# Kernel tuning notes

Measured on AMD Instinct MI355X. Metric: run time of the kernel, lower is better.

Reference implementation:

```python
import jax, jax.numpy as jnp
import numpy as np

N, E, F, H, C, K = 50000, 1600000, 128, 64, 40, 4


def setup_inputs() -> dict:
    key = jax.random.key(0)
    ks = jax.random.split(key, 4)
    x = jax.random.normal(ks[0], (N, F), dtype=jnp.float32)
    edge_index = jax.random.randint(ks[1], (2, E), 0, N, dtype=jnp.int32)
    edge_weight = jnp.ones((E,), dtype=jnp.float32)
    # lin of ChebConv: Linear(K*in, out); kaiming for layer1, xavier-ish for layer2
    W1 = jax.random.normal(ks[2], (K * F, H), dtype=jnp.float32) * (2.0 / (K * F)) ** 0.5
    b1 = jnp.zeros((H,), jnp.float32)
    W2 = jax.random.normal(ks[3], (K * H, C), dtype=jnp.float32) * (2.0 / (K * H + C)) ** 0.5
    b2 = jnp.zeros((C,), jnp.float32)
    return {"x": x, "edge_index": edge_index, "edge_weight": edge_weight,
            "W1": W1, "b1": b1, "W2": W2, "b2": b2}


def _cheb_norm(edge_index, edge_weight, num_nodes):
    """Edge weights of L_hat = 2*L/lambda_max - I with sym norm, lambda_max=2.
    L = I - D^{-1/2} A D^{-1/2}; so L_hat off-diag = -d_i^{-1/2} w d_j^{-1/2},
    diag = (1 if deg>0 else 0) - 1."""
    src, dst = edge_index[0], edge_index[1]
    deg = jax.ops.segment_sum(edge_weight, src, num_segments=num_nodes)
    dis = jnp.where(deg > 0, jax.lax.rsqrt(jnp.maximum(deg, 1e-12)), 0.0)
    w_norm = -dis[src] * edge_weight * dis[dst]   # [E] off-diagonal of L_hat
    diag = jnp.where(deg > 0, 0.0, -1.0)          # [N] diagonal of L_hat
    return src, dst, w_norm, diag


def _cheb_conv(x, src, dst, w_norm, diag, W, b, num_nodes):
    def prop(h):  # L_hat @ h via gather-multiply-scatter
        msg = w_norm[:, None] * h[src]                                  # [E, F]
        return diag[:, None] * h + jax.ops.segment_sum(msg, dst, num_segments=num_nodes)

    Tx_prev2 = x
    Tx_prev1 = prop(x)
    Txs = [Tx_prev2, Tx_prev1]
    for _ in range(2, K):
        Tx = 2.0 * prop(Tx_prev1) - Tx_prev2
        Txs.append(Tx)
        Tx_prev2, Tx_prev1 = Tx_prev1, Tx
    Z = jnp.concatenate(Txs, axis=1)              # [N, K*F]
    return Z @ W + b


def reference(x, edge_index, edge_weight, W1, b1, W2, b2):
    num_nodes = x.shape[0]
    src, dst, w_norm, diag = _cheb_norm(edge_index, edge_weight, num_nodes)
    # dropout layers are identity at inference
    h = _cheb_conv(x, src, dst, w_norm, diag, W1, b1, num_nodes)
    h = jax.nn.relu(h)
    out = _cheb_conv(h, src, dst, w_norm, diag, W2, b2, num_nodes)
    return out
```

## Files before the change

### kernel.cpp

```cpp
#include <hip/hip_runtime.h>

#define NN 50000
#define EE 1600000
#define FF 128
#define HH 64
#define CC 40
#define NB 196

#define NCH 64
#define CHE (EE / NCH)
#define NSL 4
#define SLN (NN / NSL)
#define NCHF 16
#define CHEF (EE / NCHF)
#define NSLF 16
#define SLNF (NN / NSLF)

static __device__ __forceinline__ float bf2f(unsigned short u) {
    union { unsigned int i; float f; } c; c.i = ((unsigned int)u) << 16; return c.f;
}
static __device__ __forceinline__ unsigned short f2bf(float x) {
    union { float f; unsigned int i; } c; c.f = x;
    unsigned int r = c.i + 0x7FFFu + ((c.i >> 16) & 1u);
    return (unsigned short)(r >> 16);
}

__global__ __launch_bounds__(1024) void hist_kernel(
    const int* __restrict__ src, const int* __restrict__ dst,
    const float* __restrict__ w,
    float* __restrict__ pdeg, unsigned short* __restrict__ pcnt64) {
    __shared__ float        ldeg[SLN];
    __shared__ unsigned int lcnt[SLN / 2];
    int s = blockIdx.x % NSL;
    int c = blockIdx.x / NSL;
    int base = s * SLN;
    for (int i = threadIdx.x; i < SLN; i += 1024) ldeg[i] = 0.f;
    for (int i = threadIdx.x; i < SLN / 2; i += 1024) lcnt[i] = 0u;
    __syncthreads();
    int e0 = c * CHE;
    for (int e = e0 + threadIdx.x; e < e0 + CHE; e += 1024) {
        int se = src[e], de = dst[e];
        unsigned us = (unsigned)(se - base), ud = (unsigned)(de - base);
        if (us < SLN) atomicAdd(&ldeg[us], w[e]);
        if (ud < SLN) atomicAdd(&lcnt[ud >> 1], 1u << (16 * (ud & 1)));
    }
    __syncthreads();
    for (int i = threadIdx.x; i < SLN; i += 1024) {
        pdeg[(size_t)c * NN + base + i] = ldeg[i];
        pcnt64[(size_t)c * NN + base + i] =
            (unsigned short)((lcnt[i >> 1] >> (16 * (i & 1))) & 0xFFFFu);
    }
}

__global__ void reduce_kernel(const float* __restrict__ pdeg,
                              const unsigned short* __restrict__ pcnt64,
                              int* __restrict__ pcnt16, int* __restrict__ cnt,
                              float* __restrict__ dis, float* __restrict__ diag) {
    int n = blockIdx.x * blockDim.x + threadIdx.x;
    if (n >= NN) return;
    float dsum = 0.f;
    for (int c = 0; c < NCH; ++c) dsum += pdeg[(size_t)c * NN + n];
    int run = 0;
    for (int c16 = 0; c16 < NCHF; ++c16) {
        pcnt16[(size_t)c16 * NN + n] = run;
        #pragma unroll
        for (int q = 0; q < 4; ++q)
            run += pcnt64[(size_t)(c16 * 4 + q) * NN + n];
    }
    cnt[n] = run;
    dis[n]  = (dsum > 0.f) ? rsqrtf(fmaxf(dsum, 1e-12f)) : 0.f;
    diag[n] = (dsum > 0.f) ? 0.f : -1.f;
}

__global__ void scanA_kernel(const int* __restrict__ cnt, int* __restrict__ bsum) {
    __shared__ int sh[256];
    int i = blockIdx.x * 256 + threadIdx.x;
    sh[threadIdx.x] = (i < NN) ? cnt[i] : 0;
    __syncthreads();
    for (int off = 128; off > 0; off >>= 1) {
        if (threadIdx.x < off) sh[threadIdx.x] += sh[threadIdx.x + off];
        __syncthreads();
    }
    if (threadIdx.x == 0) bsum[blockIdx.x] = sh[0];
}

__global__ void scanB_kernel(const int* __restrict__ bsum, int* __restrict__ boff,
                             int* __restrict__ row_start) {
    if (threadIdx.x == 0) {
        int run = 0;
        for (int b = 0; b < NB; ++b) { boff[b] = run; run += bsum[b]; }
        row_start[NN] = run;
    }
}

__global__ void scanC_kernel(const int* __restrict__ cnt, const int* __restrict__ boff,
                             int* __restrict__ row_start) {
    __shared__ int sh[256];
    int t = threadIdx.x;
    int i = blockIdx.x * 256 + t;
    int v = (i < NN) ? cnt[i] : 0;
    sh[t] = v;
    __syncthreads();
    for (int off = 1; off < 256; off <<= 1) {
        int x = (t >= off) ? sh[t - off] : 0;
        __syncthreads();
        sh[t] += x;
        __syncthreads();
    }
    if (i < NN) row_start[i] = boff[blockIdx.x] + sh[t] - v;
}

__global__ __launch_bounds__(1024) void fill_kernel(
    const int* __restrict__ src, const int* __restrict__ dst,
    const float* __restrict__ w, const float* __restrict__ dis,
    const int* __restrict__ row_start, const int* __restrict__ pcnt16,
    unsigned int* __restrict__ csr) {
    __shared__ unsigned int lcur[(SLNF + 1) / 2];
    int s = blockIdx.x % NSLF;
    int c = blockIdx.x / NSLF;
    int base = s * SLNF;
    for (int i = threadIdx.x; i < (SLNF + 1) / 2; i += 1024) lcur[i] = 0u;
    __syncthreads();
    int e0 = c * CHEF;
    for (int e = e0 + threadIdx.x; e < e0 + CHEF; e += 1024) {
        int de = dst[e];
        unsigned ud = (unsigned)(de - base);
        if (ud < SLNF) {
            int se = src[e];
            unsigned sh = 16 * (ud & 1);
            unsigned old = atomicAdd(&lcur[ud >> 1], 1u << sh);
            int off = (int)((old >> sh) & 0xFFFFu);
            int pos = row_start[de] + pcnt16[(size_t)c * NN + de] + off;
            float wn = -dis[se] * w[e] * dis[de];
            unsigned int entry = (unsigned)se | ((unsigned)f2bf(wn) << 16);
            __builtin_nontemporal_store(entry, csr + pos);
        }
    }
}

template <int FACT, typename OUT_T>
__global__ __launch_bounds__(256) void prop2_kernel(
    const unsigned short* __restrict__ a, int aStride, float alphaL,
    const float* __restrict__ p1, float beta1,
    const float* __restrict__ p2, float beta2, int pStride,
    const float* __restrict__ bias, int doRelu, int FOUT, int outStride,
    const float* __restrict__ diag, const int* __restrict__ rs,
    const unsigned int* __restrict__ csr, OUT_T* __restrict__ out) {
    int lane = threadIdx.x & 63;
    int wave = threadIdx.x >> 6;
    int n = blockIdx.x * 4 + wave;
    int f = lane;
    float acc = 0.f;
    if (f < FACT) {
        acc = diag[n] * bf2f(a[(size_t)n * aStride + f]);
        int j0 = rs[n], j1 = rs[n + 1];
        int j = j0;
        for (; j + 8 <= j1; j += 8) {
            unsigned cw[8];
            #pragma unroll
            for (int u = 0; u < 8; ++u) cw[u] = csr[j + u];
            float v[8];
            #pragma unroll
            for (int u = 0; u < 8; ++u)
                v[u] = bf2f(a[(size_t)(cw[u] & 0xFFFFu) * aStride + f]);
            #pragma unroll
            for (int u = 0; u < 8; ++u)
                acc = fmaf(bf2f((unsigned short)(cw[u] >> 16)), v[u], acc);
        }
        for (; j < j1; ++j) {
            unsigned cw = csr[j];
            acc = fmaf(bf2f((unsigned short)(cw >> 16)),
                       bf2f(a[(size_t)(cw & 0xFFFFu) * aStride + f]), acc);
        }
    }
    if (f < FOUT) {
        float r = alphaL * acc + beta1 * p1[(size_t)n * pStride + f];
        if (beta2 != 0.f) r = fmaf(beta2, p2[(size_t)n * pStride + f], r);
        if (bias) r += bias[f];
        if (doRelu) r = fmaxf(r, 0.f);
        OUT_T o;
        if constexpr (sizeof(OUT_T) == 2) o = f2bf(r); else o = r;
        out[(size_t)n * outStride + f] = o;
    }
}

__global__ __launch_bounds__(256) void gemm1_kernel(
    const float* __restrict__ x, const float* __restrict__ W,
    float* __restrict__ Yf, unsigned short* __restrict__ y3b) {
    __shared__ float As[64][36];
    __shared__ float Bs[32][64];
    int t = threadIdx.x;
    int m0 = blockIdx.x * 64;
    int ct = blockIdx.y;
    int tr = t / 16, tc = t % 16;
    int kq = t % 8,  ms = t / 8;
    int jb = t % 16, fb = t / 16;
    float acc[4][4] = {};
    for (int kb = 0; kb < 4; ++kb) {
        __syncthreads();
        #pragma unroll
        for (int p = 0; p < 2; ++p) {
            int m = ms + 32 * p;
            int row = m0 + m;
            float4 vv = make_float4(0.f, 0.f, 0.f, 0.f);
            if (row < NN) vv = *(const float4*)(x + (size_t)row * FF + kb * 32 + kq * 4);
            *(float4*)&As[m][kq * 4] = vv;
        }
        const float* Wb = W + ((size_t)ct * 128 + kb * 32) * HH;
        #pragma unroll
        for (int p = 0; p < 2; ++p) {
            int fi = fb + 16 * p;
            float4 vv = *(const float4*)(Wb + fi * HH + jb * 4);
            *(float4*)&Bs[fi][jb * 4] = vv;
        }
        __syncthreads();
        #pragma unroll 8
        for (int k = 0; k < 32; ++k) {
            float a0 = As[tr * 4 + 0][k], a1 = As[tr * 4 + 1][k];
            float a2 = As[tr * 4 + 2][k], a3 = As[tr * 4 + 3][k];
            float4 b = *(float4*)&Bs[k][tc * 4];
            acc[0][0] = fmaf(a0, b.x, acc[0][0]); acc[0][1] = fmaf(a0, b.y, acc[0][1]);
            acc[0][2] = fmaf(a0, b.z, acc[0][2]); acc[0][3] = fmaf(a0, b.w, acc[0][3]);
            acc[1][0] = fmaf(a1, b.x, acc[1][0]); acc[1][1] = fmaf(a1, b.y, acc[1][1]);
            acc[1][2] = fmaf(a1, b.z, acc[1][2]); acc[1][3] = fmaf(a1, b.w, acc[1][3]);
            acc[2][0] = fmaf(a2, b.x, acc[2][0]); acc[2][1] = fmaf(a2, b.y, acc[2][1]);
            acc[2][2] = fmaf(a2, b.z, acc[2][2]); acc[2][3] = fmaf(a2, b.w, acc[2][3]);
            acc[3][0] = fmaf(a3, b.x, acc[3][0]); acc[3][1] = fmaf(a3, b.y, acc[3][1]);
            acc[3][2] = fmaf(a3, b.z, acc[3][2]); acc[3][3] = fmaf(a3, b.w, acc[3][3]);
        }
    }
    #pragma unroll
    for (int r = 0; r < 4; ++r) {
        int n = m0 + tr * 4 + r;
        if (n < NN) {
            *(float4*)(Yf + (size_t)n * 256 + ct * 64 + tc * 4) =
                make_float4(acc[r][0], acc[r][1], acc[r][2], acc[r][3]);
            if (ct == 3) {
                ushort4 u4;
                u4.x = f2bf(acc[r][0]); u4.y = f2bf(acc[r][1]);
                u4.z = f2bf(acc[r][2]); u4.w = f2bf(acc[r][3]);
                *(ushort4*)(y3b + (size_t)n * 64 + tc * 4) = u4;
            }
        }
    }
}

__global__ __launch_bounds__(256) void gemm2_kernel(
    const float* __restrict__ h, const float* __restrict__ W,
    float* __restrict__ Y2f, unsigned short* __restrict__ y3b2) {
    __shared__ float As[128][36];
    __shared__ float Bs[32][40];
    int t = threadIdx.x;
    int m0 = blockIdx.x * 128;
    int kt = blockIdx.y;
    int tr = t / 8, tc = t % 8;
    int kq = t % 8, ms = t / 8;
    float acc[4][5] = {};
    for (int kb = 0; kb < 2; ++kb) {
        __syncthreads();
        #pragma unroll
        for (int p = 0; p < 4; ++p) {
            int m = ms + 32 * p;
            int row = m0 + m;
            float4 vv = make_float4(0.f, 0.f, 0.f, 0.f);
            if (row < NN) vv = *(const float4*)(h + (size_t)row * HH + kb * 32 + kq * 4);
            *(float4*)&As[m][kq * 4] = vv;
        }
        const float* Wb = W + ((size_t)kt * 64 + kb * 32) * CC;
        for (int i = t; i < 32 * CC; i += 256) ((float*)Bs)[i] = Wb[i];
        __syncthreads();
        #pragma unroll 4
        for (int k = 0; k < 32; ++k) {
            float a0 = As[tr * 4 + 0][k], a1 = As[tr * 4 + 1][k];
            float a2 = As[tr * 4 + 2][k], a3 = As[tr * 4 + 3][k];
            #pragma unroll
            for (int c = 0; c < 5; ++c) {
                float b = Bs[k][tc * 5 + c];
                acc[0][c] = fmaf(a0, b, acc[0][c]);
                acc[1][c] = fmaf(a1, b, acc[1][c]);
                acc[2][c] = fmaf(a2, b, acc[2][c]);
                acc[3][c] = fmaf(a3, b, acc[3][c]);
            }
        }
    }
    #pragma unroll
    for (int r = 0; r < 4; ++r) {
        int n = m0 + tr * 4 + r;
        if (n < NN) {
            float* orow = Y2f + (size_t)n * 256 + kt * 64;
            #pragma unroll
            for (int c = 0; c < 5; ++c) orow[tc * 5 + c] = acc[r][c];
            if (tc < 6) {
                #pragma unroll
                for (int c = 0; c < 4; ++c) orow[40 + tc * 4 + c] = 0.f;
            }
            if (kt == 3) {
                unsigned short* brow = y3b2 + (size_t)n * 64;
                #pragma unroll
                for (int c = 0; c < 5; ++c) brow[tc * 5 + c] = f2bf(acc[r][c]);
                if (tc < 6) {
                    #pragma unroll
                    for (int c = 0; c < 4; ++c) brow[40 + tc * 4 + c] = 0;
                }
            }
        }
    }
}

extern "C" void kernel_launch(void* const* d_in, const int* in_sizes, int n_in,
                              void* d_out, int out_size, void* d_ws, size_t ws_size,
                              hipStream_t stream) {
    const float* x    = (const float*)d_in[0];
    const int*   eidx = (const int*)d_in[1];
    const float* ew   = (const float*)d_in[2];
    const float* W1   = (const float*)d_in[3];
    const float* b1   = (const float*)d_in[4];
    const float* W2   = (const float*)d_in[5];
    const float* b2   = (const float*)d_in[6];
    float* out = (float*)d_out;

    const int* src = eidx;
    const int* dst = eidx + EE;

    float* p = (float*)d_ws;
    unsigned int* csr = (unsigned int*)p;  p += (size_t)EE;
    float* dis  = p;                  p += ((NN + 63) / 64) * 64;
    float* diag = p;                  p += ((NN + 63) / 64) * 64;
    float* Yf   = p;                  p += (size_t)NN * 256;
    unsigned short* y3b = (unsigned short*)p;  p += (size_t)NN * 32;
    unsigned short* u   = (unsigned short*)p;  p += (size_t)NN * 32;
    unsigned short* v   = (unsigned short*)p;  p += (size_t)NN * 32;
    float* h    = p;                  p += (size_t)NN * 64;
    int* cnt       = (int*)p;
    int* row_start = cnt + NN;
    int* bsum      = row_start + NN + 1;
    int* boff      = bsum + NB;

    float* pdeg            = Yf;
    unsigned short* pcnt64 = (unsigned short*)(Yf + (size_t)64 * NN);
    int* pcnt16            = (int*)(Yf + (size_t)96 * NN);
    float* Y2f = Yf;
    unsigned short* y3b2 = y3b;
    unsigned short* u2 = u;
    unsigned short* v2 = v;

    const int B = 256;
    hist_kernel<<<NCH * NSL, 1024, 0, stream>>>(src, dst, ew, pdeg, pcnt64);
    reduce_kernel<<<(NN + B - 1) / B, B, 0, stream>>>(pdeg, pcnt64, pcnt16, cnt, dis, diag);
    scanA_kernel<<<NB, 256, 0, stream>>>(cnt, bsum);
    scanB_kernel<<<1, 64, 0, stream>>>(bsum, boff, row_start);
    scanC_kernel<<<NB, 256, 0, stream>>>(cnt, boff, row_start);
    fill_kernel<<<NCHF * NSLF, 1024, 0, stream>>>(src, dst, ew, dis, row_start, pcnt16, csr);

    int pgrid = NN / 4;

    gemm1_kernel<<<dim3((NN + 63) / 64, 4), 256, 0, stream>>>(x, W1, Yf, y3b);
    prop2_kernel<64, unsigned short><<<pgrid, 256, 0, stream>>>(
        y3b, 64, 4.f, Yf + 128, 2.f, nullptr, 0.f, 256,
        nullptr, 0, 64, 64, diag, row_start, csr, u);
    prop2_kernel<64, unsigned short><<<pgrid, 256, 0, stream>>>(
        u, 64, 1.f, Yf + 64, 1.f, Yf + 192, -3.f, 256,
        nullptr, 0, 64, 64, diag, row_start, csr, v);
    prop2_kernel<64, float><<<pgrid, 256, 0, stream>>>(
        v, 64, 1.f, Yf, 1.f, Yf + 128, -1.f, 256,
        b1, 1, 64, 64, diag, row_start, csr, h);

    gemm2_kernel<<<dim3((NN + 127) / 128, 4), 256, 0, stream>>>(h, W2, Y2f, y3b2);
    prop2_kernel<48, unsigned short><<<pgrid, 256, 0, stream>>>(
        y3b2, 64, 4.f, Y2f + 128, 2.f, nullptr, 0.f, 256,
        nullptr, 0, 48, 64, diag, row_start, csr, u2);
    prop2_kernel<48, unsigned short><<<pgrid, 256, 0, stream>>>(
        u2, 64, 1.f, Y2f + 64, 1.f, Y2f + 192, -3.f, 256,
        nullptr, 0, 48, 64, diag, row_start, csr, v2);
    prop2_kernel<48, float><<<pgrid, 256, 0, stream>>>(
        v2, 64, 1.f, Y2f, 1.f, Y2f + 128, -1.f, 256,
        b2, 0, 40, 40, diag, row_start, csr, out);
}
```

Before: 582.3 us.

## Build CSR via two-pass bucket sort instead of sliced histogram and fill

Replaces the CSR construction with a two-pass bucket sort. The old path had a dst-count histogram, a three-kernel global scan and a sliced fill that re-read the whole edge list once per node slice. Now the degree histogram handles only src weights. A bucketA pass reads each edge once, computes its normalized bf16 weight and appends it to a fixed-capacity bucket keyed by edge partition and destination slice. A small scan then produces slice offsets, and bucketB builds per-node row starts and scatters the entries into CSR using shared-memory atomics. This removes the repeated edge-list reads, but bucket capacity is fixed at 64 entries, which relies on destinations being spread fairly evenly, and it adds an extra 8-byte-per-edge intermediate buffer.

```diff
diff --git a/kernel.cpp b/kernel.cpp
--- a/kernel.cpp
+++ b/kernel.cpp
@@ -5,16 +5,17 @@
 #define FF 128
 #define HH 64
 #define CC 40
-#define NB 196
 
 #define NCH 64
 #define CHE (EE / NCH)
 #define NSL 4
 #define SLN (NN / NSL)
-#define NCHF 16
-#define CHEF (EE / NCHF)
-#define NSLF 16
-#define SLNF (NN / NSLF)
+
+#define PA 250
+#define EPP (EE / PA)
+#define SB 250
+#define SLNB 200
+#define BCAP 64
 
 static __device__ __forceinline__ float bf2f(unsigned short u) {
     union { unsigned int i; float f; } c; c.i = ((unsigned int)u) << 16; return c.f;
@@ -25,81 +26,65 @@
     return (unsigned short)(r >> 16);
 }
 
-__global__ __launch_bounds__(1024) void hist_kernel(
-    const int* __restrict__ src, const int* __restrict__ dst,
-    const float* __restrict__ w,
-    float* __restrict__ pdeg, unsigned short* __restrict__ pcnt64) {
-    __shared__ float        ldeg[SLN];
-    __shared__ unsigned int lcnt[SLN / 2];
+__global__ __launch_bounds__(1024) void deg_hist_kernel(
+    const int* __restrict__ src, const float* __restrict__ w,
+    float* __restrict__ pdeg) {
+    __shared__ float ldeg[SLN];
     int s = blockIdx.x % NSL;
     int c = blockIdx.x / NSL;
     int base = s * SLN;
     for (int i = threadIdx.x; i < SLN; i += 1024) ldeg[i] = 0.f;
-    for (int i = threadIdx.x; i < SLN / 2; i += 1024) lcnt[i] = 0u;
     __syncthreads();
     int e0 = c * CHE;
     for (int e = e0 + threadIdx.x; e < e0 + CHE; e += 1024) {
-        int se = src[e], de = dst[e];
-        unsigned us = (unsigned)(se - base), ud = (unsigned)(de - base);
+        int se = src[e];
+        unsigned us = (unsigned)(se - base);
         if (us < SLN) atomicAdd(&ldeg[us], w[e]);
-        if (ud < SLN) atomicAdd(&lcnt[ud >> 1], 1u << (16 * (ud & 1)));
-    }
-    __syncthreads();
-    for (int i = threadIdx.x; i < SLN; i += 1024) {
+    }
+    __syncthreads();
+    for (int i = threadIdx.x; i < SLN; i += 1024)
         pdeg[(size_t)c * NN + base + i] = ldeg[i];
-        pcnt64[(size_t)c * NN + base + i] =
-            (unsigned short)((lcnt[i >> 1] >> (16 * (i & 1))) & 0xFFFFu);
-    }
 }
 
 __global__ void reduce_kernel(const float* __restrict__ pdeg,
-                              const unsigned short* __restrict__ pcnt64,
-                              int* __restrict__ pcnt16, int* __restrict__ cnt,
                               float* __restrict__ dis, float* __restrict__ diag) {
     int n = blockIdx.x * blockDim.x + threadIdx.x;
     if (n >= NN) return;
     float dsum = 0.f;
     for (int c = 0; c < NCH; ++c) dsum += pdeg[(size_t)c * NN + n];
-    int run = 0;
-    for (int c16 = 0; c16 < NCHF; ++c16) {
-        pcnt16[(size_t)c16 * NN + n] = run;
-        #pragma unroll
-        for (int q = 0; q < 4; ++q)
-            run += pcnt64[(size_t)(c16 * 4 + q) * NN + n];
-    }
-    cnt[n] = run;
     dis[n]  = (dsum > 0.f) ? rsqrtf(fmaxf(dsum, 1e-12f)) : 0.f;
     diag[n] = (dsum > 0.f) ? 0.f : -1.f;
 }
 
-__global__ void scanA_kernel(const int* __restrict__ cnt, int* __restrict__ bsum) {
-    __shared__ int sh[256];
-    int i = blockIdx.x * 256 + threadIdx.x;
-    sh[threadIdx.x] = (i < NN) ? cnt[i] : 0;
-    __syncthreads();
-    for (int off = 128; off > 0; off >>= 1) {
-        if (threadIdx.x < off) sh[threadIdx.x] += sh[threadIdx.x + off];
-        __syncthreads();
-    }
-    if (threadIdx.x == 0) bsum[blockIdx.x] = sh[0];
-}
-
-__global__ void scanB_kernel(const int* __restrict__ bsum, int* __restrict__ boff,
-                             int* __restrict__ row_start) {
-    if (threadIdx.x == 0) {
-        int run = 0;
-        for (int b = 0; b < NB; ++b) { boff[b] = run; run += bsum[b]; }
-        row_start[NN] = run;
-    }
-}
-
-__global__ void scanC_kernel(const int* __restrict__ cnt, const int* __restrict__ boff,
-                             int* __restrict__ row_start) {
+__global__ __launch_bounds__(256) void bucketA_kernel(
+    const int* __restrict__ src, const int* __restrict__ dst,
+    const float* __restrict__ w, const float* __restrict__ dis,
+    uint2* __restrict__ buckets, int* __restrict__ counts) {
+    __shared__ int lcnt[SB];
+    int p = blockIdx.x;
+    for (int i = threadIdx.x; i < SB; i += 256) lcnt[i] = 0;
+    __syncthreads();
+    int e0 = p * EPP;
+    for (int e = e0 + threadIdx.x; e < e0 + EPP; e += 256) {
+        int de = dst[e], se = src[e];
+        int sl = de / SLNB;
+        int dl = de - sl * SLNB;
+        float wn = -dis[se] * w[e] * dis[de];
+        unsigned lo = (unsigned)se | ((unsigned)f2bf(wn) << 16);
+        int idx = atomicAdd(&lcnt[sl], 1);
+        buckets[((size_t)p * SB + sl) * BCAP + idx] = make_uint2(lo, (unsigned)dl);
+    }
+    __syncthreads();
+    for (int i = threadIdx.x; i < SB; i += 256) counts[p * SB + i] = lcnt[i];
+}
+
+__global__ void scanS_kernel(const int* __restrict__ counts, int* __restrict__ sbase) {
     __shared__ int sh[256];
     int t = threadIdx.x;
-    int i = blockIdx.x * 256 + t;
-    int v = (i < NN) ? cnt[i] : 0;
-    sh[t] = v;
+    int total = 0;
+    if (t < SB)
+        for (int p = 0; p < PA; ++p) total += counts[p * SB + t];
+    sh[t] = total;
     __syncthreads();
     for (int off = 1; off < 256; off <<= 1) {
         int x = (t >= off) ? sh[t - off] : 0;
@@ -107,33 +92,52 @@
         sh[t] += x;
         __syncthreads();
     }
-    if (i < NN) row_start[i] = boff[blockIdx.x] + sh[t] - v;
-}
-
-__global__ __launch_bounds__(1024) void fill_kernel(
-    const int* __restrict__ src, const int* __restrict__ dst,
-    const float* __restrict__ w, const float* __restrict__ dis,
-    const int* __restrict__ row_start, const int* __restrict__ pcnt16,
-    unsigned int* __restrict__ csr) {
-    __shared__ unsigned int lcur[(SLNF + 1) / 2];
-    int s = blockIdx.x % NSLF;
-    int c = blockIdx.x / NSLF;
-    int base = s * SLNF;
-    for (int i = threadIdx.x; i < (SLNF + 1) / 2; i += 1024) lcur[i] = 0u;
-    __syncthreads();
-    int e0 = c * CHEF;
-    for (int e = e0 + threadIdx.x; e < e0 + CHEF; e += 1024) {
-        int de = dst[e];
-        unsigned ud = (unsigned)(de - base);
-        if (ud < SLNF) {
-            int se = src[e];
-            unsigned sh = 16 * (ud & 1);
-            unsigned old = atomicAdd(&lcur[ud >> 1], 1u << sh);
-            int off = (int)((old >> sh) & 0xFFFFu);
-            int pos = row_start[de] + pcnt16[(size_t)c * NN + de] + off;
-            float wn = -dis[se] * w[e] * dis[de];
-            unsigned int entry = (unsigned)se | ((unsigned)f2bf(wn) << 16);
-            __builtin_nontemporal_store(entry, csr + pos);
+    if (t < SB) sbase[t] = sh[t] - total;
+    if (t == SB - 1) sbase[SB] = sh[t];
+}
+
+__global__ __launch_bounds__(256) void bucketB_kernel(
+    const uint2* __restrict__ buckets, const int* __restrict__ counts,
+    const int* __restrict__ sbase,
+    int* __restrict__ row_start, unsigned int* __restrict__ csr) {
+    __shared__ int lhist[SLNB];
+    __shared__ int sh[256];
+    int s = blockIdx.x;
+    int t = threadIdx.x;
+    int lane = t & 63, wave = t >> 6;
+    for (int i = t; i < SLNB; i += 256) lhist[i] = 0;
+    __syncthreads();
+    for (int p = wave; p < PA; p += 4) {
+        int c = counts[p * SB + s];
+        const uint2* b = buckets + ((size_t)p * SB + s) * BCAP;
+        for (int i = lane; i < c; i += 64)
+            atomicAdd(&lhist[b[i].y], 1);
+    }
+    __syncthreads();
+    int v = (t < SLNB) ? lhist[t] : 0;
+    sh[t] = v;
+    __syncthreads();
+    for (int off = 1; off < 256; off <<= 1) {
+        int x = (t >= off) ? sh[t - off] : 0;
+        __syncthreads();
+        sh[t] += x;
+        __syncthreads();
+    }
+    int base = sbase[s];
+    if (t < SLNB) {
+        int excl = sh[t] - v;
+        row_start[s * SLNB + t] = base + excl;
+        lhist[t] = base + excl;
+    }
+    if (s == SB - 1 && t == 0) row_start[NN] = sbase[SB];
+    __syncthreads();
+    for (int p = wave; p < PA; p += 4) {
+        int c = counts[p * SB + s];
+        const uint2* b = buckets + ((size_t)p * SB + s) * BCAP;
+        for (int i = lane; i < c; i += 64) {
+            uint2 en = b[i];
+            int pos = atomicAdd(&lhist[en.y], 1);
+            csr[pos] = en.x;
         }
     }
 }
@@ -331,26 +335,23 @@
     unsigned short* u   = (unsigned short*)p;  p += (size_t)NN * 32;
     unsigned short* v   = (unsigned short*)p;  p += (size_t)NN * 32;
     float* h    = p;                  p += (size_t)NN * 64;
-    int* cnt       = (int*)p;
-    int* row_start = cnt + NN;
-    int* bsum      = row_start + NN + 1;
-    int* boff      = bsum + NB;
-
-    float* pdeg            = Yf;
-    unsigned short* pcnt64 = (unsigned short*)(Yf + (size_t)64 * NN);
-    int* pcnt16            = (int*)(Yf + (size_t)96 * NN);
+    int* row_start = (int*)p;
+    int* counts    = row_start + NN + 1;
+    int* sbase     = counts + PA * SB;
+
+    float* pdeg    = Yf;
+    uint2* buckets = (uint2*)(Yf + (size_t)64 * NN);
     float* Y2f = Yf;
     unsigned short* y3b2 = y3b;
     unsigned short* u2 = u;
     unsigned short* v2 = v;
 
     const int B = 256;
-    hist_kernel<<<NCH * NSL, 1024, 0, stream>>>(src, dst, ew, pdeg, pcnt64);
-    reduce_kernel<<<(NN + B - 1) / B, B, 0, stream>>>(pdeg, pcnt64, pcnt16, cnt, dis, diag);
-    scanA_kernel<<<NB, 256, 0, stream>>>(cnt, bsum);
-    scanB_kernel<<<1, 64, 0, stream>>>(bsum, boff, row_start);
-    scanC_kernel<<<NB, 256, 0, stream>>>(cnt, boff, row_start);
-    fill_kernel<<<NCHF * NSLF, 1024, 0, stream>>>(src, dst, ew, dis, row_start, pcnt16, csr);
+    deg_hist_kernel<<<NCH * NSL, 1024, 0, stream>>>(src, ew, pdeg);
+    reduce_kernel<<<(NN + B - 1) / B, B, 0, stream>>>(pdeg, dis, diag);
+    bucketA_kernel<<<PA, 256, 0, stream>>>(src, dst, ew, dis, buckets, counts);
+    scanS_kernel<<<1, 256, 0, stream>>>(counts, sbase);
+    bucketB_kernel<<<SB, 256, 0, stream>>>(buckets, counts, sbase, row_start, csr);
 
     int pgrid = NN / 4;
 
```

Measured after the change: 575.5 us. No clear change (-1.2%).
